# Performance work log

Hardware: AMD Instinct MI355X
Metric: run time of the kernel (lower is better)

The kernel has to match this reference:

```python
import jax, jax.numpy as jnp
import numpy as np

B, D, H, NC = 262144, 7, 128, 35
SQRT7 = float(np.sqrt(7.0))
W_TORSION, W_VOLUME = 1.0, 1.0  # scheduler.get_weights(epoch)


def setup_inputs() -> dict:
    key = jax.random.key(0)
    k0, k1, k2, k3 = jax.random.split(key, 4)
    coords = jax.random.normal(k0, (B, D), jnp.float32)
    # symmetric, near-identity metric (eigvalsh assumes symmetry; det ~ 1)
    A = 0.1 * jax.random.normal(k1, (B, D, D), jnp.float32)
    metric = jnp.eye(D, dtype=jnp.float32) + 0.5 * (A + jnp.swapaxes(A, -1, -2))
    W1 = jax.random.normal(k2, (D, H), jnp.float32) / np.sqrt(D)
    b1 = jnp.zeros((H,), jnp.float32)
    W2 = jax.random.normal(k3, (H, NC), jnp.float32) / np.sqrt(H)
    b2 = jnp.zeros((NC,), jnp.float32)
    return {"coords": coords, "metric": metric, "W1": W1, "b1": b1, "W2": W2, "b2": b2}


def _phi_single(c, W1, b1, W2, b2):
    # phi network: coords[7] -> 35-component 3-form
    return jnp.tanh(c @ W1 + b1) @ W2 + b2


def _hodge_single(phi, m):
    det_g = jnp.linalg.det(m)
    vol = jnp.sqrt(jnp.abs(det_g) + 1e-10)
    pd = phi * vol
    return pd / (jnp.linalg.norm(pd) + 1e-8) * SQRT7


def reference(coords, metric, W1, b1, W2, b2):
    phi = jnp.tanh(coords @ W1 + b1) @ W2 + b2  # [B,35]

    # --- torsion loss: fused per-sample Jacobians replace the 70 autograd.grad calls ---
    jac_phi = jax.vmap(jax.jacfwd(_phi_single), in_axes=(0, None, None, None, None))(
        coords, W1, b1, W2, b2)  # [B,35,7]
    d_phi_sq = jnp.sum(jnp.linalg.norm(jac_phi, axis=-1) ** 2, axis=1)  # [B]

    def phi_dual_fn(c, m):
        return _hodge_single(_phi_single(c, W1, b1, W2, b2), m)

    jac_dual = jax.vmap(jax.jacfwd(phi_dual_fn))(coords, metric)  # [B,35,7]
    d_dual_sq = jnp.sum(jnp.linalg.norm(jac_dual, axis=-1) ** 2, axis=1)
    l_torsion = d_phi_sq.mean() + d_dual_sq.mean()

    # --- volume loss ---
    det_g = jnp.linalg.det(metric)
    l_volume = jnp.mean((det_g - 1.0) ** 2)

    # --- phi normalization ---
    phi_norm_sq = jnp.sum(phi ** 2, axis=1)
    l_norm = jnp.mean((phi_norm_sq - 7.0) ** 2)

    # --- metric positivity ---
    eig = jnp.linalg.eigvalsh(metric)  # [B,7]
    l_pos = jnp.mean(jax.nn.relu(1e-6 - eig) ** 2)

    return W_TORSION * l_torsion + W_VOLUME * l_volume + l_norm + l_pos
```

## Files before the change

### kernel.cpp

```cpp
#include <hip/hip_runtime.h>

typedef _Float16 f16;
typedef f16 f16x2 __attribute__((ext_vector_type(2)));
typedef f16 f16x8 __attribute__((ext_vector_type(8)));
typedef float f32x4 __attribute__((ext_vector_type(4)));
typedef unsigned int u32;
typedef u32 u32x2 __attribute__((ext_vector_type(2)));
typedef u32 u32x4 __attribute__((ext_vector_type(4)));

#define B_TOTAL 262144
#define NBLK    512
#define TPW     4

#define OFF_QP   0
#define OFF_M2P  8704
#define OFF_W1ZT 17408
#define OFF_W1H  17920
#define OFF_W2B  19008
#define IDX_C2   19136
#define NW_U32   19140

static __device__ inline u32 pkrtz(float a, float b) {
  auto r = __builtin_amdgcn_cvt_pkrtz(a, b);
  return __builtin_bit_cast(u32, r);
}
static __device__ inline float lo16f(u32 x) { f16x2 h = __builtin_bit_cast(f16x2, x); return (float)h[0]; }
static __device__ inline float hi16f(u32 x) { f16x2 h = __builtin_bit_cast(f16x2, x); return (float)h[1]; }
static __device__ inline f16x8 frag4(const u32 v[4]) {
  u32x4 t = { v[0], v[1], v[2], v[3] };
  return __builtin_bit_cast(f16x8, t);
}
static __device__ inline f16x8 fragv(u32x4 v) { return __builtin_bit_cast(f16x8, v); }
static __device__ inline f32x4 mfma16(f16x8 a, f16x8 b, f32x4 c) {
  return __builtin_amdgcn_mfma_f32_16x16x32_f16(a, b, c, 0, 0, 0);
}
static __device__ inline float fdot2f(u32 a, u32 b, float c) {
  return __builtin_amdgcn_fdot2(__builtin_bit_cast(f16x2, a),
                                __builtin_bit_cast(f16x2, b), c, false);
}

static __device__ __host__ inline int frag_remap(int o) {
  return (o < 8) ? (4*(o >> 1) + (o & 1)) : (4*((o - 8) >> 1) + 2 + (o & 1));
}

__device__ __noinline__ void eig7_fallback(const float* Mg, float* det_o, float* lpos_o) {
  float a[49];
  for (int i = 0; i < 49; ++i) a[i] = Mg[i];
  for (int sw = 0; sw < 10; ++sw)
    for (int p = 0; p < 6; ++p)
      for (int q = p + 1; q < 7; ++q) {
        float apq = a[p*7+q];
        if (fabsf(apq) < 1e-12f) continue;
        float th = 0.5f*(a[q*7+q] - a[p*7+p]) / apq;
        float tt = 1.0f/(fabsf(th) + sqrtf(th*th + 1.0f));
        if (th < 0.0f) tt = -tt;
        float cc = 1.0f/sqrtf(tt*tt + 1.0f), ss = tt*cc;
        for (int i = 0; i < 7; ++i) {
          float aip = a[i*7+p], aiq = a[i*7+q];
          a[i*7+p] = cc*aip - ss*aiq; a[i*7+q] = ss*aip + cc*aiq;
        }
        for (int i = 0; i < 7; ++i) {
          float api = a[p*7+i], aqi = a[q*7+i];
          a[p*7+i] = cc*api - ss*aqi; a[q*7+i] = ss*api + cc*aqi;
        }
      }
  float det = 1.0f, lp = 0.0f;
  for (int i = 0; i < 7; ++i) {
    float e = a[i*7+i];
    det *= e;
    float rl = fmaxf(1e-6f - e, 0.0f);
    lp += rl*rl;
  }
  *det_o = det; *lpos_o = lp * (1.0f/7.0f);
}

__global__ void g2_prep(const float* __restrict__ W1, const float* __restrict__ b1,
                        const float* __restrict__ W2, const float* __restrict__ b2,
                        u32* __restrict__ ws) {
  int gid = blockIdx.x * 256 + threadIdx.x;
  if (gid < 8192) {
    int h = gid >> 6, kp = gid & 63, k = 2 * kp;
    float m2a = 0.f, m2b = 0.f;
    for (int x = 0; x < 35; ++x) {
      float wh = W2[h*35 + x];
      m2a = fmaf(wh, W2[k*35 + x],     m2a);
      m2b = fmaf(wh, W2[(k+1)*35 + x], m2b);
    }
    float n1a = 0.f, n1b = 0.f;
    for (int j = 0; j < 7; ++j) {
      float wj = W1[j*128 + h];
      n1a = fmaf(wj, W1[j*128 + k],   n1a);
      n1b = fmaf(wj, W1[j*128 + k+1], n1b);
    }
    int kk = kp >> 4, o = kp & 15;
    int kpn = kk*16 + frag_remap(o);
    ws[OFF_QP  + h*68 + kpn] = pkrtz(m2a*n1a, m2b*n1b);
    ws[OFF_M2P + h*68 + kpn] = pkrtz(m2a, m2b);
  } else if (gid < 8704) {
    int idx = gid - 8192, h = idx >> 2, jp = idx & 3;
    int j0 = 2*jp, j1 = 2*jp + 1;
    float a = (j0 < 7) ? W1[j0*128 + h] : b1[h];
    float b = (j1 < 7) ? W1[j1*128 + h] : b1[h];
    ws[OFF_W1ZT + h*4 + jp] = pkrtz(a, b);
  } else if (gid < 9792) {
    int idx = gid - 8704, j = idx / 68, kp = idx - j*68;
    float a = 0.f, b = 0.f;
    if (j < 7 && kp < 64) { a = W1[j*128 + 2*kp]; b = W1[j*128 + 2*kp + 1]; }
    int kpn = kp;
    if (kp < 64) { int kk = kp >> 4, o = kp & 15; kpn = kk*16 + frag_remap(o); }
    ws[OFF_W1H + j*68 + kpn] = pkrtz(a, b);
  } else if (gid < 9920) {
    int h = gid - 9792;
    float s = 0.f;
    for (int x = 0; x < 35; ++x) s = fmaf(W2[h*35 + x], b2[x], s);
    ws[OFF_W2B + h] = __builtin_bit_cast(u32, s);
  } else if (gid == 9920) {
    float s = 0.f;
    for (int x = 0; x < 35; ++x) s = fmaf(b2[x], b2[x], s);
    ws[IDX_C2] = __builtin_bit_cast(u32, s);
  }
}

__global__ __launch_bounds__(512, 2) void g2_main(
    const float* __restrict__ coords, const float* __restrict__ metric,
    const u32* __restrict__ wsW, float* __restrict__ partials) {
  __shared__ __align__(16) u32 SMEM[NW_U32];
  const int tid = threadIdx.x;

  {
    const u32x4* src = (const u32x4*)wsW;
    u32x4* dst = (u32x4*)SMEM;
    #pragma unroll
    for (int i = 0; i < 10; ++i) {
      int idx = tid + 512 * i;
      if (idx < 4785) dst[idx] = src[idx];
    }
  }
  __syncthreads();

  const int lane = tid & 63, wv = tid >> 6;
  const int g = lane >> 4, c = lane & 15;
  const int wave_gid = blockIdx.x * 8 + wv;
  const int sbase = wave_gid * 64;
  const char* LB = (const char*)SMEM;
  const float c2v = ((const float*)SMEM)[IDX_C2];

  float detv = 1.f, lposv = 0.f;
  {
    const float* Mg = metric + (size_t)(sbase + lane) * 49;
    float m[28];
    #pragma unroll
    for (int i = 0; i < 7; ++i)
      #pragma unroll
      for (int j = 0; j <= i; ++j)
        m[i*(i+1)/2 + j] = Mg[i*7 + j];
    float minpiv = 3.4e38f;
    #pragma unroll
    for (int k = 0; k < 7; ++k) {
      float piv = m[k*(k+1)/2 + k];
      minpiv = fminf(minpiv, piv);
      detv *= piv;
      float inv = 1.0f / piv;
      #pragma unroll
      for (int i = k + 1; i < 7; ++i) {
        float f = m[i*(i+1)/2 + k] * inv;
        #pragma unroll
        for (int j = k + 1; j <= i; ++j)
          m[i*(i+1)/2 + j] = fmaf(-f, m[j*(j+1)/2 + k], m[i*(i+1)/2 + j]);
      }
    }
    if (!(minpiv > 1e-4f)) eig7_fallback(Mg, &detv, &lposv);
  }

  float acc = 0.f;

  #pragma unroll 1
  for (int t = 0; t < TPW; ++t) {
    const int sb = sbase + t * 16;

    u32 bc[4] = {0,0,0,0};
    if (g < 2) {
      const float* cg = coords + (size_t)(sb + c) * 7 + 4*g;
      float f0 = cg[0], f1 = cg[1], f2 = cg[2];
      float f3 = (g == 0) ? cg[3] : 1.0f;
      bc[0] = pkrtz(f0, f1); bc[1] = pkrtz(f2, f3);
    }
    const f16x8 bfrag = frag4(bc);

    u32 sf_[4][4], tf_[4][4];
    float w2t = 0.f;
    #pragma unroll 2
    for (int mt = 0; mt < 8; ++mt) {
      u32 az[4] = {0,0,0,0};
      if (g < 2) {
        u32x2 lo = *(const u32x2*)(LB + OFF_W1ZT*4 + (16*mt + c)*16 + 8*g);
        az[0] = lo.x; az[1] = lo.y;
      }
      f32x4 zz = mfma16(frag4(az), bfrag, f32x4{0.f,0.f,0.f,0.f});
      f32x4 wb = *(const f32x4*)(LB + OFF_W2B*4 + (16*mt + 4*g)*4);
      float tt[4], ss[4];
      #pragma unroll
      for (int r = 0; r < 4; ++r) {
        float ex = __builtin_amdgcn_exp2f(zz[r] * 2.8853900817779268f);
        float rc = __builtin_amdgcn_rcpf(ex + 1.0f);
        float tv = fmaf(-2.0f, rc, 1.0f);
        tt[r] = tv; ss[r] = fmaf(-tv, tv, 1.0f);
        w2t = fmaf(tv, wb[r], w2t);
      }
      const int kk = mt >> 1, u0 = 2*(mt & 1);
      tf_[kk][u0]   = pkrtz(tt[0], tt[1]);
      tf_[kk][u0+1] = pkrtz(tt[2], tt[3]);
      sf_[kk][u0]   = pkrtz(ss[0], ss[1]);
      sf_[kk][u0+1] = pkrtz(ss[2], ss[3]);
    }

    float F2 = 0.f;
    #pragma unroll 2
    for (int mt = 0; mt < 8; ++mt) {
      const int row = c + 16*mt;
      f32x4 a = {0.f,0.f,0.f,0.f};
      #pragma unroll
      for (int kk = 0; kk < 4; ++kk) {
        u32x4 fr = *(const u32x4*)(LB + (OFF_QP + row*68 + kk*16)*4 + g*16);
        a = mfma16(fragv(fr), frag4(sf_[kk]), a);
      }
      const int kk2 = mt >> 1, u0 = 2*(mt & 1);
      F2 = fdot2f(sf_[kk2][u0],   pkrtz(a[0], a[1]), F2);
      F2 = fdot2f(sf_[kk2][u0+1], pkrtz(a[2], a[3]), F2);
    }

    float n2d = 0.f;
    f32x4 ga = {0.f,0.f,0.f,0.f};
    u32 up0 = 0, up1 = 0;
    #pragma unroll 2
    for (int mt = 0; mt < 8; ++mt) {
      const int row = c + 16*mt;
      f32x4 a = {0.f,0.f,0.f,0.f};
      #pragma unroll
      for (int kk = 0; kk < 4; ++kk) {
        u32x4 fr = *(const u32x4*)(LB + (OFF_M2P + row*68 + kk*16)*4 + g*16);
        a = mfma16(fragv(fr), frag4(tf_[kk]), a);
      }
      const int kk2 = mt >> 1, u0 = 2*(mt & 1);
      n2d = fdot2f(tf_[kk2][u0],   pkrtz(a[0], a[1]), n2d);
      n2d = fdot2f(tf_[kk2][u0+1], pkrtz(a[2], a[3]), n2d);
      f32x4 wb = *(const f32x4*)(LB + OFF_W2B*4 + (16*mt + 4*g)*4);
      float s0 = lo16f(sf_[kk2][u0]),   s1 = hi16f(sf_[kk2][u0]);
      float s2 = lo16f(sf_[kk2][u0+1]), s3 = hi16f(sf_[kk2][u0+1]);
      u32 pa = pkrtz(s0*(a[0]+wb[0]), s1*(a[1]+wb[1]));
      u32 pb = pkrtz(s2*(a[2]+wb[2]), s3*(a[3]+wb[3]));
      if ((mt & 1) == 0) {
        up0 = pa; up1 = pb;
      } else {
        const int kk = mt >> 1;
        u32 ub[4] = { up0, up1, pa, pb };
        u32x4 fr = *(const u32x4*)(LB + (OFF_W1H + c*68 + kk*16)*4 + g*16);
        ga = mfma16(fragv(fr), frag4(ub), ga);
      }
    }
    float p2g = 0.f;
    if (g == 0)      p2g = ga[0]*ga[0] + ga[1]*ga[1] + ga[2]*ga[2] + ga[3]*ga[3];
    else if (g == 1) p2g = ga[0]*ga[0] + ga[1]*ga[1] + ga[2]*ga[2];

    F2  += __shfl_xor(F2, 16);  F2  += __shfl_xor(F2, 32);
    n2d += __shfl_xor(n2d, 16); n2d += __shfl_xor(n2d, 32);
    w2t += __shfl_xor(w2t, 16); w2t += __shfl_xor(w2t, 32);
    p2g += __shfl_xor(p2g, 16); p2g += __shfl_xor(p2g, 32);

    const float det  = __shfl(detv,  16*t + c);
    const float lpos = __shfl(lposv, 16*t + c);

    if (g == 0) {
      float n2 = n2d + 2.0f*w2t + c2v;
      float v  = sqrtf(fabsf(det) + 1e-10f);
      float nn = sqrtf(fmaxf(n2, 0.0f));
      float rr = fmaf(v, nn, 1e-8f);
      float a2 = 7.0f * v * v / (rr * rr);
      float be = v / (rr * nn + 1e-20f);
      float fac = be * (2.0f - be * n2);
      float dual = a2 * (F2 - fac * p2g);
      float dm1 = det - 1.0f, nm7 = n2 - 7.0f;
      acc += F2 + dual + dm1*dm1 + nm7*nm7 + lpos;
    }
  }

  __syncthreads();
  float* SFw = (float*)SMEM;
  SFw[tid] = acc;
  __syncthreads();
  #pragma unroll
  for (int s = 256; s > 0; s >>= 1) {
    if (tid < s) SFw[tid] += SFw[tid + s];
    __syncthreads();
  }
  if (tid == 0) partials[blockIdx.x] = SFw[0];
}

__global__ void g2_finish(const float* __restrict__ partials, float* __restrict__ out) {
  __shared__ float red[256];
  int t = threadIdx.x;
  red[t] = partials[t] + partials[t + 256];
  __syncthreads();
  #pragma unroll
  for (int s = 128; s > 0; s >>= 1) {
    if (t < s) red[t] += red[t + s];
    __syncthreads();
  }
  if (t == 0) out[0] = red[0] * (1.0f / (float)B_TOTAL);
}

extern "C" void kernel_launch(void* const* d_in, const int* in_sizes, int n_in,
                              void* d_out, int out_size, void* d_ws, size_t ws_size,
                              hipStream_t stream) {
  (void)in_sizes; (void)n_in; (void)out_size; (void)ws_size;
  const float* coords = (const float*)d_in[0];
  const float* metric = (const float*)d_in[1];
  const float* W1     = (const float*)d_in[2];
  const float* b1     = (const float*)d_in[3];
  const float* W2     = (const float*)d_in[4];
  const float* b2     = (const float*)d_in[5];
  float* out = (float*)d_out;

  u32* ws = (u32*)d_ws;
  float* partials = (float*)(ws + NW_U32);

  g2_prep<<<39, 256, 0, stream>>>(W1, b1, W2, b2, ws);
  g2_main<<<NBLK, 512, 0, stream>>>(coords, metric, ws, partials);
  g2_finish<<<1, 256, 0, stream>>>(partials, out);
}
```

Baseline: 59.04 us.

## Switch main kernel from 16x16x32 to 32x32x16 MFMA tiles

Rewrites the per-wave compute to process 32 samples per tile with 32x32x16 f16 MFMA instructions instead of 16 samples with 16x16x32, halving the tile loop count. The weight workspace is repacked by the prep kernel into lane-ordered fragment layout so each lane loads a contiguous 16-byte fragment, replacing the padded row-stride layout. It also recomputes the tanh-derivative values from the tanh values instead of unpacking them, and cuts the cross-lane reductions from two shuffles to one. In exchange, each lane holds larger 16-element accumulators and twice as many fragment registers, which raises register pressure and may reduce occupancy.

```diff
diff --git a/kernel.cpp b/kernel.cpp
--- a/kernel.cpp
+++ b/kernel.cpp
@@ -4,21 +4,22 @@
 typedef f16 f16x2 __attribute__((ext_vector_type(2)));
 typedef f16 f16x8 __attribute__((ext_vector_type(8)));
 typedef float f32x4 __attribute__((ext_vector_type(4)));
+typedef float f32x16 __attribute__((ext_vector_type(16)));
 typedef unsigned int u32;
 typedef u32 u32x2 __attribute__((ext_vector_type(2)));
 typedef u32 u32x4 __attribute__((ext_vector_type(4)));
 
 #define B_TOTAL 262144
 #define NBLK    512
-#define TPW     4
+#define TPW     2
 
 #define OFF_QP   0
-#define OFF_M2P  8704
-#define OFF_W1ZT 17408
-#define OFF_W1H  17920
-#define OFF_W2B  19008
-#define IDX_C2   19136
-#define NW_U32   19140
+#define OFF_M2P  8192
+#define OFF_W1H  16384
+#define OFF_W1ZT 18432
+#define OFF_W2B  18944
+#define IDX_C2   19072
+#define NW_U32   19076
 
 static __device__ inline u32 pkrtz(float a, float b) {
   auto r = __builtin_amdgcn_cvt_pkrtz(a, b);
@@ -31,17 +32,14 @@
   return __builtin_bit_cast(f16x8, t);
 }
 static __device__ inline f16x8 fragv(u32x4 v) { return __builtin_bit_cast(f16x8, v); }
-static __device__ inline f32x4 mfma16(f16x8 a, f16x8 b, f32x4 c) {
-  return __builtin_amdgcn_mfma_f32_16x16x32_f16(a, b, c, 0, 0, 0);
+static __device__ inline f32x16 mfma32(f16x8 a, f16x8 b, f32x16 c) {
+  return __builtin_amdgcn_mfma_f32_32x32x16_f16(a, b, c, 0, 0, 0);
 }
 static __device__ inline float fdot2f(u32 a, u32 b, float c) {
   return __builtin_amdgcn_fdot2(__builtin_bit_cast(f16x2, a),
                                 __builtin_bit_cast(f16x2, b), c, false);
 }
-
-static __device__ __host__ inline int frag_remap(int o) {
-  return (o < 8) ? (4*(o >> 1) + (o & 1)) : (4*((o - 8) >> 1) + 2 + (o & 1));
-}
+static __device__ __host__ inline int kl(int w, int g) { return (w & 3) + 8 * (w >> 2) + 4 * g; }
 
 __device__ __noinline__ void eig7_fallback(const float* Mg, float* det_o, float* lpos_o) {
   float a[49];
@@ -79,42 +77,50 @@
                         u32* __restrict__ ws) {
   int gid = blockIdx.x * 256 + threadIdx.x;
   if (gid < 8192) {
-    int h = gid >> 6, kp = gid & 63, k = 2 * kp;
+    int frag = gid >> 8;
+    int lane = (gid >> 2) & 63, w2 = gid & 3;
+    int mt = frag >> 3, kk = frag & 7;
+    int g = lane >> 5, row = 32*mt + (lane & 31);
+    int k0 = 16*kk + kl(2*w2,     g);
+    int k1 = 16*kk + kl(2*w2 + 1, g);
     float m2a = 0.f, m2b = 0.f;
     for (int x = 0; x < 35; ++x) {
-      float wh = W2[h*35 + x];
-      m2a = fmaf(wh, W2[k*35 + x],     m2a);
-      m2b = fmaf(wh, W2[(k+1)*35 + x], m2b);
+      float wh = W2[row*35 + x];
+      m2a = fmaf(wh, W2[k0*35 + x], m2a);
+      m2b = fmaf(wh, W2[k1*35 + x], m2b);
     }
     float n1a = 0.f, n1b = 0.f;
     for (int j = 0; j < 7; ++j) {
-      float wj = W1[j*128 + h];
-      n1a = fmaf(wj, W1[j*128 + k],   n1a);
-      n1b = fmaf(wj, W1[j*128 + k+1], n1b);
-    }
-    int kk = kp >> 4, o = kp & 15;
-    int kpn = kk*16 + frag_remap(o);
-    ws[OFF_QP  + h*68 + kpn] = pkrtz(m2a*n1a, m2b*n1b);
-    ws[OFF_M2P + h*68 + kpn] = pkrtz(m2a, m2b);
-  } else if (gid < 8704) {
-    int idx = gid - 8192, h = idx >> 2, jp = idx & 3;
-    int j0 = 2*jp, j1 = 2*jp + 1;
-    float a = (j0 < 7) ? W1[j0*128 + h] : b1[h];
+      float wj = W1[j*128 + row];
+      n1a = fmaf(wj, W1[j*128 + k0], n1a);
+      n1b = fmaf(wj, W1[j*128 + k1], n1b);
+    }
+    ws[OFF_QP  + gid] = pkrtz(m2a*n1a, m2b*n1b);
+    ws[OFF_M2P + gid] = pkrtz(m2a, m2b);
+  } else if (gid < 10240) {
+    int idx = gid - 8192;
+    int kk = idx >> 8, lane = (idx >> 2) & 63, w2 = idx & 3;
+    int g = lane >> 5, j = lane & 31;
+    float a = 0.f, b = 0.f;
+    if (j < 7) {
+      a = W1[j*128 + 16*kk + kl(2*w2,     g)];
+      b = W1[j*128 + 16*kk + kl(2*w2 + 1, g)];
+    }
+    ws[OFF_W1H + idx] = pkrtz(a, b);
+  } else if (gid < 10752) {
+    int idx = gid - 10240;
+    int mt = idx >> 7, r = idx & 127, lane = r >> 1, half = r & 1;
+    int g = lane >> 5, h = 32*mt + (lane & 31);
+    int j0 = 4*g + 2*half, j1 = j0 + 1;
+    float a = W1[j0*128 + h];
     float b = (j1 < 7) ? W1[j1*128 + h] : b1[h];
-    ws[OFF_W1ZT + h*4 + jp] = pkrtz(a, b);
-  } else if (gid < 9792) {
-    int idx = gid - 8704, j = idx / 68, kp = idx - j*68;
-    float a = 0.f, b = 0.f;
-    if (j < 7 && kp < 64) { a = W1[j*128 + 2*kp]; b = W1[j*128 + 2*kp + 1]; }
-    int kpn = kp;
-    if (kp < 64) { int kk = kp >> 4, o = kp & 15; kpn = kk*16 + frag_remap(o); }
-    ws[OFF_W1H + j*68 + kpn] = pkrtz(a, b);
-  } else if (gid < 9920) {
-    int h = gid - 9792;
+    ws[OFF_W1ZT + mt*128 + lane*2 + half] = pkrtz(a, b);
+  } else if (gid < 10880) {
+    int h = gid - 10752;
     float s = 0.f;
     for (int x = 0; x < 35; ++x) s = fmaf(W2[h*35 + x], b2[x], s);
     ws[OFF_W2B + h] = __builtin_bit_cast(u32, s);
-  } else if (gid == 9920) {
+  } else if (gid == 10880) {
     float s = 0.f;
     for (int x = 0; x < 35; ++x) s = fmaf(b2[x], b2[x], s);
     ws[IDX_C2] = __builtin_bit_cast(u32, s);
@@ -133,13 +139,13 @@
     #pragma unroll
     for (int i = 0; i < 10; ++i) {
       int idx = tid + 512 * i;
-      if (idx < 4785) dst[idx] = src[idx];
+      if (idx < 4769) dst[idx] = src[idx];
     }
   }
   __syncthreads();
 
   const int lane = tid & 63, wv = tid >> 6;
-  const int g = lane >> 4, c = lane & 15;
+  const int g = lane >> 5, cs = lane & 31;
   const int wave_gid = blockIdx.x * 8 + wv;
   const int sbase = wave_gid * 64;
   const char* LB = (const char*)SMEM;
@@ -176,111 +182,110 @@
 
   #pragma unroll 1
   for (int t = 0; t < TPW; ++t) {
-    const int sb = sbase + t * 16;
-
-    u32 bc[4] = {0,0,0,0};
-    if (g < 2) {
-      const float* cg = coords + (size_t)(sb + c) * 7 + 4*g;
-      float f0 = cg[0], f1 = cg[1], f2 = cg[2];
-      float f3 = (g == 0) ? cg[3] : 1.0f;
-      bc[0] = pkrtz(f0, f1); bc[1] = pkrtz(f2, f3);
-    }
-    const f16x8 bfrag = frag4(bc);
-
-    u32 sf_[4][4], tf_[4][4];
+    const float* cg = coords + (size_t)(sbase + 32*t + cs) * 7;
+    u32 bcv[4] = {0,0,0,0};
+    if (g == 0) { bcv[0] = pkrtz(cg[0], cg[1]); bcv[1] = pkrtz(cg[2], cg[3]); }
+    else        { bcv[0] = pkrtz(cg[4], cg[5]); bcv[1] = pkrtz(cg[6], 1.0f); }
+    const f16x8 bfrag = frag4(bcv);
+
+    u32 sf_[8][4], tf_[8][4];
     float w2t = 0.f;
-    #pragma unroll 2
-    for (int mt = 0; mt < 8; ++mt) {
-      u32 az[4] = {0,0,0,0};
-      if (g < 2) {
-        u32x2 lo = *(const u32x2*)(LB + OFF_W1ZT*4 + (16*mt + c)*16 + 8*g);
-        az[0] = lo.x; az[1] = lo.y;
-      }
-      f32x4 zz = mfma16(frag4(az), bfrag, f32x4{0.f,0.f,0.f,0.f});
-      f32x4 wb = *(const f32x4*)(LB + OFF_W2B*4 + (16*mt + 4*g)*4);
-      float tt[4], ss[4];
-      #pragma unroll
-      for (int r = 0; r < 4; ++r) {
-        float ex = __builtin_amdgcn_exp2f(zz[r] * 2.8853900817779268f);
-        float rc = __builtin_amdgcn_rcpf(ex + 1.0f);
-        float tv = fmaf(-2.0f, rc, 1.0f);
-        tt[r] = tv; ss[r] = fmaf(-tv, tv, 1.0f);
-        w2t = fmaf(tv, wb[r], w2t);
-      }
-      const int kk = mt >> 1, u0 = 2*(mt & 1);
-      tf_[kk][u0]   = pkrtz(tt[0], tt[1]);
-      tf_[kk][u0+1] = pkrtz(tt[2], tt[3]);
-      sf_[kk][u0]   = pkrtz(ss[0], ss[1]);
-      sf_[kk][u0+1] = pkrtz(ss[2], ss[3]);
+    #pragma unroll
+    for (int mt = 0; mt < 4; ++mt) {
+      u32x2 az2 = *(const u32x2*)(LB + (OFF_W1ZT + mt*128 + lane*2) * 4);
+      u32 azv[4] = { az2.x, az2.y, 0, 0 };
+      f32x16 zz = mfma32(frag4(azv), bfrag,
+                         f32x16{0,0,0,0,0,0,0,0,0,0,0,0,0,0,0,0});
+      #pragma unroll
+      for (int q = 0; q < 4; ++q) {
+        f32x4 wb = *(const f32x4*)(LB + (OFF_W2B + 32*mt + 8*q + 4*g) * 4);
+        float tq[4], sq[4];
+        #pragma unroll
+        for (int e = 0; e < 4; ++e) {
+          float z  = zz[4*q + e];
+          float ex = __builtin_amdgcn_exp2f(z * 2.8853900817779268f);
+          float rc = __builtin_amdgcn_rcpf(ex + 1.0f);
+          float tv = fmaf(-2.0f, rc, 1.0f);
+          tq[e] = tv; sq[e] = fmaf(-tv, tv, 1.0f);
+          w2t = fmaf(tv, wb[e], w2t);
+        }
+        const int kkx = 2*mt + (q >> 1), ub = 2*(q & 1);
+        tf_[kkx][ub]   = pkrtz(tq[0], tq[1]);
+        tf_[kkx][ub+1] = pkrtz(tq[2], tq[3]);
+        sf_[kkx][ub]   = pkrtz(sq[0], sq[1]);
+        sf_[kkx][ub+1] = pkrtz(sq[2], sq[3]);
+      }
     }
 
     float F2 = 0.f;
-    #pragma unroll 2
-    for (int mt = 0; mt < 8; ++mt) {
-      const int row = c + 16*mt;
-      f32x4 a = {0.f,0.f,0.f,0.f};
-      #pragma unroll
-      for (int kk = 0; kk < 4; ++kk) {
-        u32x4 fr = *(const u32x4*)(LB + (OFF_QP + row*68 + kk*16)*4 + g*16);
-        a = mfma16(fragv(fr), frag4(sf_[kk]), a);
-      }
-      const int kk2 = mt >> 1, u0 = 2*(mt & 1);
-      F2 = fdot2f(sf_[kk2][u0],   pkrtz(a[0], a[1]), F2);
-      F2 = fdot2f(sf_[kk2][u0+1], pkrtz(a[2], a[3]), F2);
+    #pragma unroll 1
+    for (int mt = 0; mt < 4; ++mt) {
+      f32x16 a = {0,0,0,0,0,0,0,0,0,0,0,0,0,0,0,0};
+      #pragma unroll
+      for (int kk = 0; kk < 8; ++kk) {
+        u32x4 fr = *(const u32x4*)(LB + (OFF_QP + (mt*8 + kk)*256 + lane*4) * 4);
+        a = mfma32(fragv(fr), frag4(sf_[kk]), a);
+      }
+      #pragma unroll
+      for (int u = 0; u < 4; ++u) {
+        F2 = fdot2f(sf_[2*mt][u],   pkrtz(a[2*u],   a[2*u+1]), F2);
+        F2 = fdot2f(sf_[2*mt+1][u], pkrtz(a[8+2*u], a[9+2*u]), F2);
+      }
     }
 
     float n2d = 0.f;
-    f32x4 ga = {0.f,0.f,0.f,0.f};
-    u32 up0 = 0, up1 = 0;
-    #pragma unroll 2
-    for (int mt = 0; mt < 8; ++mt) {
-      const int row = c + 16*mt;
-      f32x4 a = {0.f,0.f,0.f,0.f};
-      #pragma unroll
-      for (int kk = 0; kk < 4; ++kk) {
-        u32x4 fr = *(const u32x4*)(LB + (OFF_M2P + row*68 + kk*16)*4 + g*16);
-        a = mfma16(fragv(fr), frag4(tf_[kk]), a);
-      }
-      const int kk2 = mt >> 1, u0 = 2*(mt & 1);
-      n2d = fdot2f(tf_[kk2][u0],   pkrtz(a[0], a[1]), n2d);
-      n2d = fdot2f(tf_[kk2][u0+1], pkrtz(a[2], a[3]), n2d);
-      f32x4 wb = *(const f32x4*)(LB + OFF_W2B*4 + (16*mt + 4*g)*4);
-      float s0 = lo16f(sf_[kk2][u0]),   s1 = hi16f(sf_[kk2][u0]);
-      float s2 = lo16f(sf_[kk2][u0+1]), s3 = hi16f(sf_[kk2][u0+1]);
-      u32 pa = pkrtz(s0*(a[0]+wb[0]), s1*(a[1]+wb[1]));
-      u32 pb = pkrtz(s2*(a[2]+wb[2]), s3*(a[3]+wb[3]));
-      if ((mt & 1) == 0) {
-        up0 = pa; up1 = pb;
-      } else {
-        const int kk = mt >> 1;
-        u32 ub[4] = { up0, up1, pa, pb };
-        u32x4 fr = *(const u32x4*)(LB + (OFF_W1H + c*68 + kk*16)*4 + g*16);
-        ga = mfma16(fragv(fr), frag4(ub), ga);
-      }
-    }
-    float p2g = 0.f;
-    if (g == 0)      p2g = ga[0]*ga[0] + ga[1]*ga[1] + ga[2]*ga[2] + ga[3]*ga[3];
-    else if (g == 1) p2g = ga[0]*ga[0] + ga[1]*ga[1] + ga[2]*ga[2];
-
-    F2  += __shfl_xor(F2, 16);  F2  += __shfl_xor(F2, 32);
-    n2d += __shfl_xor(n2d, 16); n2d += __shfl_xor(n2d, 32);
-    w2t += __shfl_xor(w2t, 16); w2t += __shfl_xor(w2t, 32);
-    p2g += __shfl_xor(p2g, 16); p2g += __shfl_xor(p2g, 32);
-
-    const float det  = __shfl(detv,  16*t + c);
-    const float lpos = __shfl(lposv, 16*t + c);
-
-    if (g == 0) {
+    f32x16 ga = {0,0,0,0,0,0,0,0,0,0,0,0,0,0,0,0};
+    #pragma unroll 1
+    for (int mt = 0; mt < 4; ++mt) {
+      f32x16 a = {0,0,0,0,0,0,0,0,0,0,0,0,0,0,0,0};
+      #pragma unroll
+      for (int kk = 0; kk < 8; ++kk) {
+        u32x4 fr = *(const u32x4*)(LB + (OFF_M2P + (mt*8 + kk)*256 + lane*4) * 4);
+        a = mfma32(fragv(fr), frag4(tf_[kk]), a);
+      }
+      f32x4 wbq0 = *(const f32x4*)(LB + (OFF_W2B + 32*mt +      4*g) * 4);
+      f32x4 wbq1 = *(const f32x4*)(LB + (OFF_W2B + 32*mt +  8 + 4*g) * 4);
+      f32x4 wbq2 = *(const f32x4*)(LB + (OFF_W2B + 32*mt + 16 + 4*g) * 4);
+      f32x4 wbq3 = *(const f32x4*)(LB + (OFF_W2B + 32*mt + 24 + 4*g) * 4);
+      u32 ub0[4], ub1[4];
+      #pragma unroll
+      for (int u = 0; u < 4; ++u) {
+        n2d = fdot2f(tf_[2*mt][u],   pkrtz(a[2*u],   a[2*u+1]), n2d);
+        n2d = fdot2f(tf_[2*mt+1][u], pkrtz(a[8+2*u], a[9+2*u]), n2d);
+        const int e = (2*u) & 3;
+        f32x4 wlo = (u < 2) ? wbq0 : wbq1;
+        f32x4 whi = (u < 2) ? wbq2 : wbq3;
+        float t0 = lo16f(tf_[2*mt][u]),   t1 = hi16f(tf_[2*mt][u]);
+        float s0 = fmaf(-t0, t0, 1.0f),   s1 = fmaf(-t1, t1, 1.0f);
+        ub0[u] = pkrtz(s0*(a[2*u] + wlo[e]), s1*(a[2*u+1] + wlo[e+1]));
+        float t2 = lo16f(tf_[2*mt+1][u]), t3 = hi16f(tf_[2*mt+1][u]);
+        float s2 = fmaf(-t2, t2, 1.0f),   s3 = fmaf(-t3, t3, 1.0f);
+        ub1[u] = pkrtz(s2*(a[8+2*u] + whi[e]), s3*(a[9+2*u] + whi[e+1]));
+      }
+      u32x4 f0 = *(const u32x4*)(LB + (OFF_W1H + (2*mt)*256   + lane*4) * 4);
+      ga = mfma32(fragv(f0), frag4(ub0), ga);
+      u32x4 f1 = *(const u32x4*)(LB + (OFF_W1H + (2*mt+1)*256 + lane*4) * 4);
+      ga = mfma32(fragv(f1), frag4(ub1), ga);
+    }
+    float p2g = ga[0]*ga[0] + ga[1]*ga[1] + ga[2]*ga[2];
+    if (g == 0) p2g = fmaf(ga[3], ga[3], p2g);
+
+    F2  += __shfl_xor(F2, 32);
+    n2d += __shfl_xor(n2d, 32);
+    w2t += __shfl_xor(w2t, 32);
+    p2g += __shfl_xor(p2g, 32);
+
+    if ((lane >> 5) == t) {
       float n2 = n2d + 2.0f*w2t + c2v;
-      float v  = sqrtf(fabsf(det) + 1e-10f);
+      float v  = sqrtf(fabsf(detv) + 1e-10f);
       float nn = sqrtf(fmaxf(n2, 0.0f));
       float rr = fmaf(v, nn, 1e-8f);
       float a2 = 7.0f * v * v / (rr * rr);
       float be = v / (rr * nn + 1e-20f);
       float fac = be * (2.0f - be * n2);
       float dual = a2 * (F2 - fac * p2g);
-      float dm1 = det - 1.0f, nm7 = n2 - 7.0f;
-      acc += F2 + dual + dm1*dm1 + nm7*nm7 + lpos;
+      float dm1 = detv - 1.0f, nm7 = n2 - 7.0f;
+      acc += F2 + dual + dm1*dm1 + nm7*nm7 + lposv;
     }
   }
 
@@ -324,7 +329,7 @@
   u32* ws = (u32*)d_ws;
   float* partials = (float*)(ws + NW_U32);
 
-  g2_prep<<<39, 256, 0, stream>>>(W1, b1, W2, b2, ws);
+  g2_prep<<<43, 256, 0, stream>>>(W1, b1, W2, b2, ws);
   g2_main<<<NBLK, 512, 0, stream>>>(coords, metric, ws, partials);
   g2_finish<<<1, 256, 0, stream>>>(partials, out);
 }
```

Result: slower. 77.40 us, median of 5 (+31.1%).

## Process two sample tiles per sweep sharing LDS weight fragments, pre-swizzle weights

Applied to the files above, without the earlier changes.

The main loop now handles two 16-sample tiles per iteration, so every A fragment loaded from LDS feeds two MFMAs and LDS traffic per sample is halved. The prep kernel writes the weight matrices in per-lane fragment order, which removes the padded row layout and turns each LDS read into one contiguous vector load. The sech² term is no longer kept in registers and is recomputed from tanh with packed fp16 FMAs, freeing registers and replacing fp32 multiplies with pk-mul ops. The cost is more registers for two accumulator sets and slightly different fp16 rounding in the s terms.

```diff
diff --git a/kernel.cpp b/kernel.cpp
--- a/kernel.cpp
+++ b/kernel.cpp
@@ -10,22 +10,20 @@
 
 #define B_TOTAL 262144
 #define NBLK    512
-#define TPW     4
+#define SWEEPS  2
 
 #define OFF_QP   0
-#define OFF_M2P  8704
-#define OFF_W1ZT 17408
-#define OFF_W1H  17920
-#define OFF_W2B  19008
-#define IDX_C2   19136
-#define NW_U32   19140
+#define OFF_M2P  8192
+#define OFF_W1H  16384
+#define OFF_W1Z  17408
+#define OFF_W2B  18432
+#define IDX_C2   18560
+#define NW_U32   18564
 
 static __device__ inline u32 pkrtz(float a, float b) {
   auto r = __builtin_amdgcn_cvt_pkrtz(a, b);
   return __builtin_bit_cast(u32, r);
 }
-static __device__ inline float lo16f(u32 x) { f16x2 h = __builtin_bit_cast(f16x2, x); return (float)h[0]; }
-static __device__ inline float hi16f(u32 x) { f16x2 h = __builtin_bit_cast(f16x2, x); return (float)h[1]; }
 static __device__ inline f16x8 frag4(const u32 v[4]) {
   u32x4 t = { v[0], v[1], v[2], v[3] };
   return __builtin_bit_cast(f16x8, t);
@@ -38,9 +36,18 @@
   return __builtin_amdgcn_fdot2(__builtin_bit_cast(f16x2, a),
                                 __builtin_bit_cast(f16x2, b), c, false);
 }
-
-static __device__ __host__ inline int frag_remap(int o) {
-  return (o < 8) ? (4*(o >> 1) + (o & 1)) : (4*((o - 8) >> 1) + 2 + (o & 1));
+static __device__ inline u32 s_from_t(u32 t) {
+  f16x2 tv = __builtin_bit_cast(f16x2, t);
+  f16x2 one = { (f16)1.0f, (f16)1.0f };
+  f16x2 sv = __builtin_elementwise_fma(-tv, tv, one);
+  return __builtin_bit_cast(u32, sv);
+}
+static __device__ inline u32 pkmul(u32 a, u32 b) {
+  f16x2 r = __builtin_bit_cast(f16x2, a) * __builtin_bit_cast(f16x2, b);
+  return __builtin_bit_cast(u32, r);
+}
+static __device__ inline int inv_remap(int g, int w) {
+  return ((w & 2) == 0) ? (2*g + (w & 1)) : (8 + 2*g + (w & 1));
 }
 
 __device__ __noinline__ void eig7_fallback(const float* Mg, float* det_o, float* lpos_o) {
@@ -79,42 +86,54 @@
                         u32* __restrict__ ws) {
   int gid = blockIdx.x * 256 + threadIdx.x;
   if (gid < 8192) {
-    int h = gid >> 6, kp = gid & 63, k = 2 * kp;
+    int f = gid >> 8;
+    int lane = (gid >> 2) & 63, w = gid & 3;
+    int mt = f >> 2, kk = f & 3;
+    int c = lane & 15, g = lane >> 4;
+    int h = 16*mt + c;
+    int o = inv_remap(g, w);
+    int kp = kk*16 + o, k0 = 2*kp, k1 = k0 + 1;
     float m2a = 0.f, m2b = 0.f;
     for (int x = 0; x < 35; ++x) {
       float wh = W2[h*35 + x];
-      m2a = fmaf(wh, W2[k*35 + x],     m2a);
-      m2b = fmaf(wh, W2[(k+1)*35 + x], m2b);
+      m2a = fmaf(wh, W2[k0*35 + x], m2a);
+      m2b = fmaf(wh, W2[k1*35 + x], m2b);
     }
     float n1a = 0.f, n1b = 0.f;
     for (int j = 0; j < 7; ++j) {
       float wj = W1[j*128 + h];
-      n1a = fmaf(wj, W1[j*128 + k],   n1a);
-      n1b = fmaf(wj, W1[j*128 + k+1], n1b);
-    }
-    int kk = kp >> 4, o = kp & 15;
-    int kpn = kk*16 + frag_remap(o);
-    ws[OFF_QP  + h*68 + kpn] = pkrtz(m2a*n1a, m2b*n1b);
-    ws[OFF_M2P + h*68 + kpn] = pkrtz(m2a, m2b);
-  } else if (gid < 8704) {
-    int idx = gid - 8192, h = idx >> 2, jp = idx & 3;
-    int j0 = 2*jp, j1 = 2*jp + 1;
-    float a = (j0 < 7) ? W1[j0*128 + h] : b1[h];
-    float b = (j1 < 7) ? W1[j1*128 + h] : b1[h];
-    ws[OFF_W1ZT + h*4 + jp] = pkrtz(a, b);
-  } else if (gid < 9792) {
-    int idx = gid - 8704, j = idx / 68, kp = idx - j*68;
+      n1a = fmaf(wj, W1[j*128 + k0], n1a);
+      n1b = fmaf(wj, W1[j*128 + k1], n1b);
+    }
+    ws[OFF_QP  + gid] = pkrtz(m2a*n1a, m2b*n1b);
+    ws[OFF_M2P + gid] = pkrtz(m2a, m2b);
+  } else if (gid < 9216) {
+    int idx = gid - 8192;
+    int kk = idx >> 8, lane = (idx >> 2) & 63, w = idx & 3;
+    int j = lane & 15, g = lane >> 4;
+    int o = inv_remap(g, w);
+    int kp = kk*16 + o, k0 = 2*kp, k1 = k0 + 1;
     float a = 0.f, b = 0.f;
-    if (j < 7 && kp < 64) { a = W1[j*128 + 2*kp]; b = W1[j*128 + 2*kp + 1]; }
-    int kpn = kp;
-    if (kp < 64) { int kk = kp >> 4, o = kp & 15; kpn = kk*16 + frag_remap(o); }
-    ws[OFF_W1H + j*68 + kpn] = pkrtz(a, b);
-  } else if (gid < 9920) {
-    int h = gid - 9792;
+    if (j < 7) { a = W1[j*128 + k0]; b = W1[j*128 + k1]; }
+    ws[OFF_W1H + idx] = pkrtz(a, b);
+  } else if (gid < 10240) {
+    int idx = gid - 9216;
+    int mt = idx >> 7, r = idx & 127, lane = r >> 1, half = r & 1;
+    int c = lane & 15, g = lane >> 4;
+    int h = 16*mt + c;
+    float a = 0.f, b = 0.f;
+    if (g < 2) {
+      int jp = 2*g + half, j0 = 2*jp, j1 = j0 + 1;
+      a = W1[j0*128 + h];
+      b = (j1 < 7) ? W1[j1*128 + h] : b1[h];
+    }
+    ws[OFF_W1Z + (mt*64 + lane)*2 + half] = pkrtz(a, b);
+  } else if (gid < 10368) {
+    int h = gid - 10240;
     float s = 0.f;
     for (int x = 0; x < 35; ++x) s = fmaf(W2[h*35 + x], b2[x], s);
     ws[OFF_W2B + h] = __builtin_bit_cast(u32, s);
-  } else if (gid == 9920) {
+  } else if (gid == 10368) {
     float s = 0.f;
     for (int x = 0; x < 35; ++x) s = fmaf(b2[x], b2[x], s);
     ws[IDX_C2] = __builtin_bit_cast(u32, s);
@@ -133,7 +152,7 @@
     #pragma unroll
     for (int i = 0; i < 10; ++i) {
       int idx = tid + 512 * i;
-      if (idx < 4785) dst[idx] = src[idx];
+      if (idx < 4641) dst[idx] = src[idx];
     }
   }
   __syncthreads();
@@ -175,112 +194,141 @@
   float acc = 0.f;
 
   #pragma unroll 1
-  for (int t = 0; t < TPW; ++t) {
-    const int sb = sbase + t * 16;
-
-    u32 bc[4] = {0,0,0,0};
-    if (g < 2) {
-      const float* cg = coords + (size_t)(sb + c) * 7 + 4*g;
-      float f0 = cg[0], f1 = cg[1], f2 = cg[2];
-      float f3 = (g == 0) ? cg[3] : 1.0f;
-      bc[0] = pkrtz(f0, f1); bc[1] = pkrtz(f2, f3);
-    }
-    const f16x8 bfrag = frag4(bc);
-
-    u32 sf_[4][4], tf_[4][4];
-    float w2t = 0.f;
+  for (int t = 0; t < SWEEPS; ++t) {
+    const int sb = sbase + 32*t;
+
+    const float* cgA = coords + (size_t)(sb + c) * 7;
+    const float* cgB = cgA + 16*7;
+    u32 bA[4] = {0,0,0,0}, bB[4] = {0,0,0,0};
+    if (g == 0) {
+      bA[0] = pkrtz(cgA[0], cgA[1]); bA[1] = pkrtz(cgA[2], cgA[3]);
+      bB[0] = pkrtz(cgB[0], cgB[1]); bB[1] = pkrtz(cgB[2], cgB[3]);
+    } else if (g == 1) {
+      bA[0] = pkrtz(cgA[4], cgA[5]); bA[1] = pkrtz(cgA[6], 1.0f);
+      bB[0] = pkrtz(cgB[4], cgB[5]); bB[1] = pkrtz(cgB[6], 1.0f);
+    }
+    const f16x8 bfA = frag4(bA), bfB = frag4(bB);
+
+    u32 tfa[4][4], tfb[4][4];
+    float w2ta = 0.f, w2tb = 0.f;
     #pragma unroll 2
     for (int mt = 0; mt < 8; ++mt) {
-      u32 az[4] = {0,0,0,0};
-      if (g < 2) {
-        u32x2 lo = *(const u32x2*)(LB + OFF_W1ZT*4 + (16*mt + c)*16 + 8*g);
-        az[0] = lo.x; az[1] = lo.y;
-      }
-      f32x4 zz = mfma16(frag4(az), bfrag, f32x4{0.f,0.f,0.f,0.f});
-      f32x4 wb = *(const f32x4*)(LB + OFF_W2B*4 + (16*mt + 4*g)*4);
-      float tt[4], ss[4];
-      #pragma unroll
-      for (int r = 0; r < 4; ++r) {
-        float ex = __builtin_amdgcn_exp2f(zz[r] * 2.8853900817779268f);
-        float rc = __builtin_amdgcn_rcpf(ex + 1.0f);
-        float tv = fmaf(-2.0f, rc, 1.0f);
-        tt[r] = tv; ss[r] = fmaf(-tv, tv, 1.0f);
-        w2t = fmaf(tv, wb[r], w2t);
+      u32x2 az2 = *(const u32x2*)(LB + (OFF_W1Z + (mt*64 + lane)*2) * 4);
+      u32 azv[4] = { az2.x, az2.y, 0, 0 };
+      const f16x8 afr = frag4(azv);
+      f32x4 zzA = mfma16(afr, bfA, f32x4{0.f,0.f,0.f,0.f});
+      f32x4 zzB = mfma16(afr, bfB, f32x4{0.f,0.f,0.f,0.f});
+      f32x4 wb = *(const f32x4*)(LB + (OFF_W2B + 16*mt + 4*g) * 4);
+      float tA[4], tB[4];
+      #pragma unroll
+      for (int e = 0; e < 4; ++e) {
+        float exA = __builtin_amdgcn_exp2f(zzA[e] * 2.8853900817779268f);
+        float tvA = fmaf(-2.0f, __builtin_amdgcn_rcpf(exA + 1.0f), 1.0f);
+        tA[e] = tvA; w2ta = fmaf(tvA, wb[e], w2ta);
+        float exB = __builtin_amdgcn_exp2f(zzB[e] * 2.8853900817779268f);
+        float tvB = fmaf(-2.0f, __builtin_amdgcn_rcpf(exB + 1.0f), 1.0f);
+        tB[e] = tvB; w2tb = fmaf(tvB, wb[e], w2tb);
       }
       const int kk = mt >> 1, u0 = 2*(mt & 1);
-      tf_[kk][u0]   = pkrtz(tt[0], tt[1]);
-      tf_[kk][u0+1] = pkrtz(tt[2], tt[3]);
-      sf_[kk][u0]   = pkrtz(ss[0], ss[1]);
-      sf_[kk][u0+1] = pkrtz(ss[2], ss[3]);
-    }
-
-    float F2 = 0.f;
+      tfa[kk][u0]   = pkrtz(tA[0], tA[1]);
+      tfa[kk][u0+1] = pkrtz(tA[2], tA[3]);
+      tfb[kk][u0]   = pkrtz(tB[0], tB[1]);
+      tfb[kk][u0+1] = pkrtz(tB[2], tB[3]);
+    }
+
+    float F2a = 0.f, F2b = 0.f;
     #pragma unroll 2
     for (int mt = 0; mt < 8; ++mt) {
-      const int row = c + 16*mt;
-      f32x4 a = {0.f,0.f,0.f,0.f};
+      f32x4 va = {0.f,0.f,0.f,0.f}, vb = {0.f,0.f,0.f,0.f};
       #pragma unroll
       for (int kk = 0; kk < 4; ++kk) {
-        u32x4 fr = *(const u32x4*)(LB + (OFF_QP + row*68 + kk*16)*4 + g*16);
-        a = mfma16(fragv(fr), frag4(sf_[kk]), a);
+        u32x4 fr = *(const u32x4*)(LB + (OFF_QP + ((mt*4 + kk)*64 + lane)*4) * 4);
+        const f16x8 qa = fragv(fr);
+        u32 sA[4], sB[4];
+        #pragma unroll
+        for (int w = 0; w < 4; ++w) { sA[w] = s_from_t(tfa[kk][w]); sB[w] = s_from_t(tfb[kk][w]); }
+        va = mfma16(qa, frag4(sA), va);
+        vb = mfma16(qa, frag4(sB), vb);
       }
       const int kk2 = mt >> 1, u0 = 2*(mt & 1);
-      F2 = fdot2f(sf_[kk2][u0],   pkrtz(a[0], a[1]), F2);
-      F2 = fdot2f(sf_[kk2][u0+1], pkrtz(a[2], a[3]), F2);
-    }
-
-    float n2d = 0.f;
-    f32x4 ga = {0.f,0.f,0.f,0.f};
-    u32 up0 = 0, up1 = 0;
+      F2a = fdot2f(s_from_t(tfa[kk2][u0]),   pkrtz(va[0], va[1]), F2a);
+      F2a = fdot2f(s_from_t(tfa[kk2][u0+1]), pkrtz(va[2], va[3]), F2a);
+      F2b = fdot2f(s_from_t(tfb[kk2][u0]),   pkrtz(vb[0], vb[1]), F2b);
+      F2b = fdot2f(s_from_t(tfb[kk2][u0+1]), pkrtz(vb[2], vb[3]), F2b);
+    }
+
+    float n2a = 0.f, n2b = 0.f;
+    f32x4 gaa = {0.f,0.f,0.f,0.f}, gab = {0.f,0.f,0.f,0.f};
+    u32 upA0 = 0, upA1 = 0, upB0 = 0, upB1 = 0;
     #pragma unroll 2
     for (int mt = 0; mt < 8; ++mt) {
-      const int row = c + 16*mt;
-      f32x4 a = {0.f,0.f,0.f,0.f};
+      f32x4 va = {0.f,0.f,0.f,0.f}, vb = {0.f,0.f,0.f,0.f};
       #pragma unroll
       for (int kk = 0; kk < 4; ++kk) {
-        u32x4 fr = *(const u32x4*)(LB + (OFF_M2P + row*68 + kk*16)*4 + g*16);
-        a = mfma16(fragv(fr), frag4(tf_[kk]), a);
+        u32x4 fr = *(const u32x4*)(LB + (OFF_M2P + ((mt*4 + kk)*64 + lane)*4) * 4);
+        const f16x8 qa = fragv(fr);
+        va = mfma16(qa, frag4(tfa[kk]), va);
+        vb = mfma16(qa, frag4(tfb[kk]), vb);
       }
       const int kk2 = mt >> 1, u0 = 2*(mt & 1);
-      n2d = fdot2f(tf_[kk2][u0],   pkrtz(a[0], a[1]), n2d);
-      n2d = fdot2f(tf_[kk2][u0+1], pkrtz(a[2], a[3]), n2d);
-      f32x4 wb = *(const f32x4*)(LB + OFF_W2B*4 + (16*mt + 4*g)*4);
-      float s0 = lo16f(sf_[kk2][u0]),   s1 = hi16f(sf_[kk2][u0]);
-      float s2 = lo16f(sf_[kk2][u0+1]), s3 = hi16f(sf_[kk2][u0+1]);
-      u32 pa = pkrtz(s0*(a[0]+wb[0]), s1*(a[1]+wb[1]));
-      u32 pb = pkrtz(s2*(a[2]+wb[2]), s3*(a[3]+wb[3]));
+      n2a = fdot2f(tfa[kk2][u0],   pkrtz(va[0], va[1]), n2a);
+      n2a = fdot2f(tfa[kk2][u0+1], pkrtz(va[2], va[3]), n2a);
+      n2b = fdot2f(tfb[kk2][u0],   pkrtz(vb[0], vb[1]), n2b);
+      n2b = fdot2f(tfb[kk2][u0+1], pkrtz(vb[2], vb[3]), n2b);
+      f32x4 wb = *(const f32x4*)(LB + (OFF_W2B + 16*mt + 4*g) * 4);
+      u32 paA = pkmul(s_from_t(tfa[kk2][u0]),   pkrtz(va[0] + wb[0], va[1] + wb[1]));
+      u32 pbA = pkmul(s_from_t(tfa[kk2][u0+1]), pkrtz(va[2] + wb[2], va[3] + wb[3]));
+      u32 paB = pkmul(s_from_t(tfb[kk2][u0]),   pkrtz(vb[0] + wb[0], vb[1] + wb[1]));
+      u32 pbB = pkmul(s_from_t(tfb[kk2][u0+1]), pkrtz(vb[2] + wb[2], vb[3] + wb[3]));
       if ((mt & 1) == 0) {
-        up0 = pa; up1 = pb;
+        upA0 = paA; upA1 = pbA; upB0 = paB; upB1 = pbB;
       } else {
         const int kk = mt >> 1;
-        u32 ub[4] = { up0, up1, pa, pb };
-        u32x4 fr = *(const u32x4*)(LB + (OFF_W1H + c*68 + kk*16)*4 + g*16);
-        ga = mfma16(fragv(fr), frag4(ub), ga);
-      }
-    }
-    float p2g = 0.f;
-    if (g == 0)      p2g = ga[0]*ga[0] + ga[1]*ga[1] + ga[2]*ga[2] + ga[3]*ga[3];
-    else if (g == 1) p2g = ga[0]*ga[0] + ga[1]*ga[1] + ga[2]*ga[2];
-
-    F2  += __shfl_xor(F2, 16);  F2  += __shfl_xor(F2, 32);
-    n2d += __shfl_xor(n2d, 16); n2d += __shfl_xor(n2d, 32);
-    w2t += __shfl_xor(w2t, 16); w2t += __shfl_xor(w2t, 32);
-    p2g += __shfl_xor(p2g, 16); p2g += __shfl_xor(p2g, 32);
-
-    const float det  = __shfl(detv,  16*t + c);
-    const float lpos = __shfl(lposv, 16*t + c);
-
-    if (g == 0) {
-      float n2 = n2d + 2.0f*w2t + c2v;
-      float v  = sqrtf(fabsf(det) + 1e-10f);
-      float nn = sqrtf(fmaxf(n2, 0.0f));
-      float rr = fmaf(v, nn, 1e-8f);
-      float a2 = 7.0f * v * v / (rr * rr);
-      float be = v / (rr * nn + 1e-20f);
-      float fac = be * (2.0f - be * n2);
-      float dual = a2 * (F2 - fac * p2g);
-      float dm1 = det - 1.0f, nm7 = n2 - 7.0f;
-      acc += F2 + dual + dm1*dm1 + nm7*nm7 + lpos;
+        u32x4 frw = *(const u32x4*)(LB + (OFF_W1H + (kk*64 + lane)*4) * 4);
+        const f16x8 wfr = fragv(frw);
+        u32 uA[4] = { upA0, upA1, paA, pbA };
+        u32 uB[4] = { upB0, upB1, paB, pbB };
+        gaa = mfma16(wfr, frag4(uA), gaa);
+        gab = mfma16(wfr, frag4(uB), gab);
+      }
+    }
+    float p2ga = gaa[0]*gaa[0] + gaa[1]*gaa[1] + gaa[2]*gaa[2];
+    float p2gb = gab[0]*gab[0] + gab[1]*gab[1] + gab[2]*gab[2];
+    if (g == 0) { p2ga = fmaf(gaa[3], gaa[3], p2ga); p2gb = fmaf(gab[3], gab[3], p2gb); }
+
+    F2a += __shfl_xor(F2a, 16); F2a += __shfl_xor(F2a, 32);
+    F2b += __shfl_xor(F2b, 16); F2b += __shfl_xor(F2b, 32);
+    n2a += __shfl_xor(n2a, 16); n2a += __shfl_xor(n2a, 32);
+    n2b += __shfl_xor(n2b, 16); n2b += __shfl_xor(n2b, 32);
+    w2ta += __shfl_xor(w2ta, 16); w2ta += __shfl_xor(w2ta, 32);
+    w2tb += __shfl_xor(w2tb, 16); w2tb += __shfl_xor(w2tb, 32);
+    p2ga += __shfl_xor(p2ga, 16); p2ga += __shfl_xor(p2ga, 32);
+    p2gb += __shfl_xor(p2gb, 16); p2gb += __shfl_xor(p2gb, 32);
+
+    const float det0 = __shfl(detv,  32*t + c);
+    const float lp0  = __shfl(lposv, 32*t + c);
+    const float det1 = __shfl(detv,  32*t + 16 + c);
+    const float lp1  = __shfl(lposv, 32*t + 16 + c);
+
+    {
+      float F2 = (g == 0) ? F2a : F2b;
+      float n2d = (g == 0) ? n2a : n2b;
+      float w2t = (g == 0) ? w2ta : w2tb;
+      float p2g = (g == 0) ? p2ga : p2gb;
+      float det = (g == 0) ? det0 : det1;
+      float lpo = (g == 0) ? lp0 : lp1;
+      if (g < 2) {
+        float n2 = n2d + 2.0f*w2t + c2v;
+        float v  = sqrtf(fabsf(det) + 1e-10f);
+        float nn = sqrtf(fmaxf(n2, 0.0f));
+        float rr = fmaf(v, nn, 1e-8f);
+        float a2 = 7.0f * v * v / (rr * rr);
+        float be = v / (rr * nn + 1e-20f);
+        float fac = be * (2.0f - be * n2);
+        float dual = a2 * (F2 - fac * p2g);
+        float dm1 = det - 1.0f, nm7 = n2 - 7.0f;
+        acc += F2 + dual + dm1*dm1 + nm7*nm7 + lpo;
+      }
     }
   }
 
@@ -324,7 +372,7 @@
   u32* ws = (u32*)d_ws;
   float* partials = (float*)(ws + NW_U32);
 
-  g2_prep<<<39, 256, 0, stream>>>(W1, b1, W2, b2, ws);
+  g2_prep<<<41, 256, 0, stream>>>(W1, b1, W2, b2, ws);
   g2_main<<<NBLK, 512, 0, stream>>>(coords, metric, ws, partials);
   g2_finish<<<1, 256, 0, stream>>>(partials, out);
 }
```

Result: faster. 51.68 us (-12.5%).
